# Kernel tuning notes

Hardware: AMD Instinct MI355X
Metric: run time of the kernel (lower is better)

The kernel has to match this reference:

```python
import jax, jax.numpy as jnp
import numpy as np

# dims
D_IN, D, H, HD = 1536, 256, 8, 32
DEPTH, FFN = 2, 1024
B, L = 1, 8191
NGRIDS, TILE = 256, 256
SEGMENTS = [1024, 2048, 4096, 8192, 16384]   # get_optimal_segment_length(32768, 256)
RATIOS = [1, 2, 4, 8, 16]                    # LongNet canonical dilation ratios
SCALE = HD ** -0.5


def setup_inputs() -> dict:
    key = jax.random.key(0)
    ks = jax.random.split(key, 16)
    w = lambda k, s: jax.random.normal(k, s, jnp.float32) * 0.02
    return {
        "x": jax.random.normal(ks[0], (B, L, D_IN), jnp.float32),
        "coords": jax.random.randint(ks[1], (B, L, 2), 0, NGRIDS * TILE, jnp.int32),
        "proj_w": w(ks[2], (D_IN, D)), "proj_b": jnp.zeros((D,), jnp.float32),
        "cls_tok": w(ks[3], (1, 1, D)),
        "Wq": w(ks[4], (DEPTH, D, D)), "Wk": w(ks[5], (DEPTH, D, D)),
        "Wv": w(ks[6], (DEPTH, D, D)), "Wo": w(ks[7], (DEPTH, D, D)),
        "bq": jnp.zeros((DEPTH, D), jnp.float32), "bk": jnp.zeros((DEPTH, D), jnp.float32),
        "bv": jnp.zeros((DEPTH, D), jnp.float32), "bo": jnp.zeros((DEPTH, D), jnp.float32),
        "ln1_g": jnp.ones((DEPTH, D), jnp.float32), "ln1_b": jnp.zeros((DEPTH, D), jnp.float32),
        "ln2_g": jnp.ones((DEPTH, D), jnp.float32), "ln2_b": jnp.zeros((DEPTH, D), jnp.float32),
        "W1": w(ks[8], (DEPTH, D, FFN)), "b1": jnp.zeros((DEPTH, FFN), jnp.float32),
        "W2": w(ks[9], (DEPTH, FFN, D)), "b2": jnp.zeros((DEPTH, D), jnp.float32),
        "enc_g": jnp.ones((D,), jnp.float32), "enc_b": jnp.zeros((D,), jnp.float32),
        "norm_g": jnp.ones((D,), jnp.float32), "norm_b": jnp.zeros((D,), jnp.float32),
    }


def _ln(x, g, b):
    mu = x.mean(-1, keepdims=True)
    v = ((x - mu) ** 2).mean(-1, keepdims=True)
    return (x - mu) * jax.lax.rsqrt(v + 1e-5) * g + b


def _pos_table():
    # MAE-style 2D sincos pos embed, row 0 = cls (zeros). [NGRIDS^2+1, D]
    g = jnp.arange(NGRIDS, dtype=jnp.float32)
    gw, gh = jnp.meshgrid(g, g)  # gw[i,j]=j, gh[i,j]=i; flatten index = i*NGRIDS + j
    def one(pos):
        omega = 1.0 / (10000.0 ** (jnp.arange(D // 4, dtype=jnp.float32) / (D // 4)))
        o = pos.reshape(-1)[:, None] * omega[None]
        return jnp.concatenate([jnp.sin(o), jnp.cos(o)], -1)
    tab = jnp.concatenate([one(gw), one(gh)], -1)
    return jnp.concatenate([jnp.zeros((1, D), jnp.float32), tab], 0)


def _dilated_attn(q, k, v):
    # q,k,v: [B,S,H,HD]. LongNet: per (segment w, dilation r) branch, sparse in-segment
    # attention on stride-r rows (head-dependent offset h%r), branches fused via their
    # softmax log-sum-exp weights.
    S = q.shape[1]
    hh = jnp.arange(H)[:, None]
    outs, lses = [], []
    for w, r in zip(SEGMENTS, RATIOS):
        n = (S + w - 1) // w
        Sp = n * w
        def seg(t):
            tp = jnp.pad(t, ((0, 0), (0, Sp - S), (0, 0), (0, 0)))
            return tp.reshape(B, n, w, H, HD).transpose(0, 1, 3, 2, 4)  # [B,n,H,w,HD]
        qs_, ks_, vs_ = seg(q), seg(k), seg(v)
        t = w // r
        idx = (hh % r) + r * jnp.arange(t)[None, :]                  # [H,t]
        qs = qs_[:, :, hh, idx]                                      # [B,n,H,t,HD]
        ks = ks_[:, :, hh, idx]
        vs = vs_[:, :, hh, idx]
        valid = (jnp.arange(n)[:, None, None] * w + idx[None]) < S   # [n,H,t]
        sc = jnp.einsum('bnhtd,bnhsd->bnhts', qs, ks) * SCALE
        sc = jnp.where(valid[None, :, :, None, :], sc, -1e9)
        m = sc.max(-1, keepdims=True)
        p = jnp.exp(sc - m)
        den = p.sum(-1, keepdims=True)
        o = jnp.einsum('bnhts,bnhsd->bnhtd', p, vs) / den
        lse = m[..., 0] + jnp.log(den[..., 0])                       # [B,n,H,t]
        fo = jnp.zeros((B, n, H, w, HD), q.dtype).at[:, :, hh, idx].set(o)
        fl = jnp.full((B, n, H, w), -1e30, q.dtype).at[:, :, hh, idx].set(lse)
        outs.append(fo.transpose(0, 1, 3, 2, 4).reshape(B, Sp, H, HD)[:, :S])
        lses.append(fl.transpose(0, 1, 3, 2).reshape(B, Sp, H)[:, :S])
    Ls = jnp.stack(lses)   # [5,B,S,H]
    Os = jnp.stack(outs)   # [5,B,S,H,HD]
    wts = jnp.exp(Ls - Ls.max(0, keepdims=True))
    return (wts[..., None] * Os).sum(0) / wts.sum(0)[..., None]


def _forward(x, coords, proj_w, proj_b, cls_tok, Wq, Wk, Wv, Wo, bq, bk, bv, bo,
             ln1_g, ln1_b, ln2_g, ln2_b, W1, b1, W2, b2, enc_g, enc_b, norm_g, norm_b):
    h = x @ proj_w + proj_b                                   # patch embed [B,L,D]
    tab = _pos_table()
    cg = jnp.floor(coords.astype(jnp.float32) / TILE).astype(jnp.int32)
    pos = cg[..., 0] * NGRIDS + cg[..., 1] + 1                # coords_to_pos
    h = h + tab[pos]
    cls = jnp.broadcast_to(cls_tok + tab[0], (B, 1, D))
    h = jnp.concatenate([cls, h], 1)                          # [B,S,D], S = L+1
    S = h.shape[1]
    for i in range(DEPTH):                                    # pre-LN LongNet encoder layers
        a = _ln(h, ln1_g[i], ln1_b[i])
        q = (a @ Wq[i] + bq[i]).reshape(B, S, H, HD)
        k = (a @ Wk[i] + bk[i]).reshape(B, S, H, HD)
        v = (a @ Wv[i] + bv[i]).reshape(B, S, H, HD)
        o = _dilated_attn(q, k, v).reshape(B, S, D)
        h = h + o @ Wo[i] + bo[i]
        f = _ln(h, ln2_g[i], ln2_b[i])
        h = h + jax.nn.gelu(f @ W1[i] + b1[i], approximate=False) @ W2[i] + b2[i]
    h = _ln(h, enc_g, enc_b)     # encoder final LN
    h = _ln(h, norm_g, norm_b)   # model self.norm
    return h[:, 0]               # cls embedding (global_pool=False)


def reference(x, coords, proj_w, proj_b, cls_tok, Wq, Wk, Wv, Wo, bq, bk, bv, bo,
              ln1_g, ln1_b, ln2_g, ln2_b, W1, b1, W2, b2, enc_g, enc_b, norm_g, norm_b):
    return _forward(x, coords, proj_w, proj_b, cls_tok, Wq, Wk, Wv, Wo, bq, bk, bv, bo,
                    ln1_g, ln1_b, ln2_g, ln2_b, W1, b1, W2, b2, enc_g, enc_b, norm_g, norm_b)
```

## Files before the change

### kernel.cpp

```cpp
#include <hip/hip_runtime.h>
#include <math.h>

#define S_TOT 8192
#define DD 256
#define NHEAD 8
#define HDSZ 32
#define ATT_SCALE 0.17677669529663687f
#define ATT_SCALE_LOG2E 0.25506601f

typedef short short8 __attribute__((ext_vector_type(8)));
typedef short short4v __attribute__((ext_vector_type(4)));
typedef float f32x4 __attribute__((ext_vector_type(4)));
typedef unsigned short ushort;

#define OFF_PROJ 0
#define OFF_WQ0  393216
#define OFF_WK0  458752
#define OFF_WV0  524288
#define OFF_WO0  589824
#define OFF_W10  655360
#define OFF_W20  917504
#define OFF_WK1  1179648
#define OFF_WV1  1245184
#define OFF_WQ1  1310720
// ... 131 lines not shown
void gemm4_kernel(const ushort* __restrict__ A, const ushort* __restrict__ Bt,
                  const float* __restrict__ bias, void* __restrict__ Cv,
                  int M, int N, int K, int flags, const int* __restrict__ coords)
{
    __shared__ ushort As[3][64][64];
    __shared__ ushort Bs[3][BN][64];
    constexpr int NT = BN / 32;
    const int nx  = N / BN;
    const int ny8 = gridDim.x / (8 * nx);
    const int b   = blockIdx.x;
    const int c8  = b & 7;
    const int j   = b >> 3;
    const int m0  = (c8 * ny8 + j / nx) * 64;
    const int n0  = (j % nx) * BN;

    const int tid  = threadIdx.x;
    const int wave = tid >> 6;
    const int lane = tid & 63;
    const int lrow = lane & 15;
    const int quad = lane >> 4;
    const int wr = (wave >> 1) * 32;
    const int wc = (wave & 1) * (BN / 2);

    float* Cf  = (float*)Cv;
    ushort* Cb = (ushort*)Cv;

    f32x4 acc[2][NT];
    #pragma unroll
    for (int mt = 0; mt < 2; ++mt)
        #pragma unroll
        for (int nt = 0; nt < NT; ++nt)
            acc[mt][nt] = (f32x4){0.f, 0.f, 0.f, 0.f};

    const int srow = tid >> 3;
    const int scol = (tid & 7) * 16;

    #define STAGE(BUF, KK)                                                        \
    do {                                                                          \
        _Pragma("unroll")                                                         \
        for (int c = 0; c < 2; ++c) {                                             \
            const int row = c * 32 + srow;                                        \
            const int sb  = scol ^ ((row & 7) << 4);                              \
            const ushort* srcp = A + (size_t)(m0 + row) * K + (KK) + (sb >> 1);   \
            __builtin_amdgcn_global_load_lds(                                     \
                (const __attribute__((address_space(1))) void*)srcp,              \
                (__attribute__((address_space(3))) void*)&As[BUF][c * 32 + wave * 8][0], \
                16, 0, 0);                                                        \
        }                                                                         \
        _Pragma("unroll")                                                         \
        for (int c = 0; c < BN / 32; ++c) {                                       \
            const int row = c * 32 + srow;                                        \
            const int sb  = scol ^ ((row & 7) << 4);                              \
            const ushort* srcp = Bt + (size_t)(n0 + row) * K + (KK) + (sb >> 1);  \
            __builtin_amdgcn_global_load_lds(                                     \
                (const __attribute__((address_space(1))) void*)srcp,              \
                (__attribute__((address_space(3))) void*)&Bs[BUF][c * 32 + wave * 8][0], \
                16, 0, 0);                                                        \
        }                                                                         \
    } while (0)

    #define COMPUTE(BUF)                                                          \
    do {                                                                          \
        _Pragma("unroll")                                                         \
        for (int ks = 0; ks < 2; ++ks) {                                          \
            short8 af[2], bfr[NT];                                                \
            _Pragma("unroll")                                                     \
            for (int mt = 0; mt < 2; ++mt) {                                      \
                const int row = wr + mt * 16 + lrow;                              \
                const int cb  = (ks * 64 + quad * 16) ^ ((row & 7) << 4);         \
                af[mt] = *(const short8*)((const char*)&As[BUF][row][0] + cb);    \
            }                                                                     \
            _Pragma("unroll")                                                     \
            for (int nt = 0; nt < NT; ++nt) {                                     \
                const int row = wc + nt * 16 + lrow;                              \
                const int cb  = (ks * 64 + quad * 16) ^ ((row & 7) << 4);         \
                bfr[nt] = *(const short8*)((const char*)&Bs[BUF][row][0] + cb);   \
            }                                                                     \
            _Pragma("unroll")                                                     \
            for (int mt = 0; mt < 2; ++mt)                                        \
                _Pragma("unroll")                                                 \
                for (int nt = 0; nt < NT; ++nt)                                   \
                    acc[mt][nt] = __builtin_amdgcn_mfma_f32_16x16x32_bf16(        \
                                      af[mt], bfr[nt], acc[mt][nt], 0, 0, 0);     \
        }                                                                         \
    } while (0)

    #define WAIT_BAR_N()                                                          \
    do {                                                                          \
        if constexpr (BN == 64) { asm volatile("s_waitcnt vmcnt(4)" ::: "memory"); } \
        else                    { asm volatile("s_waitcnt vmcnt(6)" ::: "memory"); } \
        __builtin_amdgcn_sched_barrier(0);                                        \
        __builtin_amdgcn_s_barrier();                                             \
        __builtin_amdgcn_sched_barrier(0);                                        \
    } while (0)

    #define WAIT_BAR_0()                                                          \
    do {                                                                          \
        asm volatile("s_waitcnt vmcnt(0)" ::: "memory");                          \
        __builtin_amdgcn_sched_barrier(0);                                        \
        __builtin_amdgcn_s_barrier();                                             \
        __builtin_amdgcn_sched_barrier(0);                                        \
    } while (0)

    const int ktiles = K >> 6;
    STAGE(0, 0);
    STAGE(1, 64);
    int bt = 0;
    for (int t = 0; t < ktiles - 2; ++t) {
        WAIT_BAR_N();
        const int nb = (bt + 2 >= 3) ? bt - 1 : bt + 2;
        STAGE(nb, (t + 2) * 64);
        COMPUTE(bt);
        bt = (bt + 1 == 3) ? 0 : bt + 1;
    }
    WAIT_BAR_N();
    COMPUTE(bt);
    bt = (bt + 1 == 3) ? 0 : bt + 1;
    WAIT_BAR_0();
    COMPUTE(bt);
    #undef STAGE
    #undef COMPUTE
    #undef WAIT_BAR_N
    #undef WAIT_BAR_0

    #pragma unroll
    for (int mt = 0; mt < 2; ++mt) {
        #pragma unroll
        for (int rg = 0; rg < 4; ++rg) {
            const int r = m0 + wr + mt * 16 + quad * 4 + rg;
            if (r >= M) continue;
            #pragma unroll
            for (int nt = 0; nt < NT; ++nt) {
                const int c = n0 + wc + nt * 16 + lrow;
                float vv = acc[mt][nt][rg] + bias[c];
                if (flags & 8) {
                    const int cg = coords[2 * r + ((c < 128) ? 1 : 0)] >> 8;
                    const float omega = exp2f((float)(c & 63) * -0.2076205059304703f);
                    const float o = (float)cg * omega;
                    vv += ((c & 64) == 0) ? __sinf(o) : __cosf(o);
                }
                if (flags & 16) { if (c < 256) vv *= ATT_SCALE_LOG2E; }
                if (flags & 2) vv = gelu_exact(vv);
                if (flags & 4) {
                    Cb[(size_t)r * N + c] = f2bf(vv);
                } else {
                    if (flags & 1) vv += Cf[(size_t)r * N + c];
                    Cf[(size_t)r * N + c] = vv;
                }
            }
        }
    }
}

__global__ __launch_bounds__(256)
void attn_mfma_kernel(const ushort* __restrict__ q, const ushort* __restrict__ k,
                      const ushort* __restrict__ v, float* __restrict__ bo5,
                      float* __restrict__ lse5, int qs)
{
    __shared__ ushort Kb[2][64][40];
    __shared__ ushort Vt[2][32][72];

    const int unit = blockIdx.x;
    const int segu = unit >> 3;
    const int head = unit & 7;
    int b2, n;
    if (segu < 8)        { b2 = 0; n = segu; }
    else if (segu < 12)  { b2 = 1; n = segu - 8; }
    else if (segu < 14)  { b2 = 2; n = segu - 12; }
    else if (segu == 14) { b2 = 3; n = 0; }
    else                 { b2 = 4; n = 0; }
    const int w  = 1024 << b2;
    const int rr = 1 << b2;
    const int base = n * w + (head & (rr - 1));

    int kEnd = (S_TOT - base + rr - 1) >> b2;
    if (kEnd > 1024) kEnd = 1024;
    if (blockIdx.y * 128 >= kEnd) return;

    const int tid  = threadIdx.x;
    const int wave = tid >> 6;
    const int lane = tid & 63;
    const int lrow = lane & 15;
    const int quad = lane >> 4;

    short8 qf[2];
    #pragma unroll
    for (int m = 0; m < 2; ++m) {
        const int j  = blockIdx.y * 128 + wave * 32 + m * 16 + lrow;
        const int pq = base + rr * j;
        qf[m] = *(const short8*)(q + (size_t)pq * qs + head * HDSZ + quad * 8);
    }

    f32x4 acc[2][2];
    float lsum[2] = {0.f, 0.f};
    #pragma unroll
    for (int m = 0; m < 2; ++m)
        #pragma unroll
        for (int dt = 0; dt < 2; ++dt) acc[m][dt] = (f32x4){0.f, 0.f, 0.f, 0.f};

    const int skr = tid >> 2;
    const int sdb = (tid & 3) * 8;
    const int grp = tid & 3;
    const int wcol = (2 * skr + 32 * grp) & 127;

    size_t prow = (size_t)(base + rr * skr) * qs + head * HDSZ + sdb;
    uint4 kreg = *(const uint4*)(k + prow);
    uint4 vreg = *(const uint4*)(v + prow);

    *(uint4*)&Kb[0][skr][sdb] = kreg;
    {
        const ushort* vp = (const ushort*)&vreg;
        #pragma unroll
        for (int i = 0; i < 8; ++i)
            *(ushort*)((char*)&Vt[0][sdb + i][0] + wcol) = vp[i];
    }

    int cur = 0;
    for (int kc = 0; kc < kEnd; kc += 64) {
        __syncthreads();
        const bool more = (kc + 64 < kEnd);
        if (more) {
            prow = (size_t)(base + rr * (kc + 64 + skr)) * qs + head * HDSZ + sdb;
            kreg = *(const uint4*)(k + prow);
            vreg = *(const uint4*)(v + prow);
        }

        short8 kf[4];
        #pragma unroll
        for (int t = 0; t < 4; ++t)
            kf[t] = *(const short8*)&Kb[cur][t * 16 + lrow][quad * 8];

        short8 vf[2][2];
        #pragma unroll
        for (int g = 0; g < 2; ++g)
            #pragma unroll
            for (int dt = 0; dt < 2; ++dt) {
                const int row  = dt * 16 + lrow;
                const int rotb = 32 * ((row >> 3) & 3);
                const int cb0  = (64 * g + 8 * quad + rotb) & 127;
                const int cb1  = (64 * g + 8 * quad + 32 + rotb) & 127;
                vf[g][dt] = cat44(*(const short4v*)((const char*)&Vt[cur][row][0] + cb0),
                                  *(const short4v*)((const char*)&Vt[cur][row][0] + cb1));
            }

        #pragma unroll
        for (int m = 0; m < 2; ++m) {
            f32x4 sc[4];
            #pragma unroll
            for (int t = 0; t < 4; ++t)
                sc[t] = __builtin_amdgcn_mfma_f32_16x16x32_bf16(
                            kf[t], qf[m], (f32x4){0.f,0.f,0.f,0.f}, 0, 0, 0);
            float p[4][4];
            #pragma unroll
            for (int t = 0; t < 4; ++t)
                #pragma unroll
                for (int rg = 0; rg < 4; ++rg)
                    p[t][rg] = exp2f(sc[t][rg]);
            float ps = 0.f;
            #pragma unroll
            for (int t = 0; t < 4; ++t)
                ps += (p[t][0] + p[t][1]) + (p[t][2] + p[t][3]);
            lsum[m] += ps;
            unsigned pw[4][2];
            #pragma unroll
            for (int t = 0; t < 4; ++t) {
                pw[t][0] = cvtpk_bf16(p[t][0], p[t][1]);
                pw[t][1] = cvtpk_bf16(p[t][2], p[t][3]);
            }
            #pragma unroll
            for (int g = 0; g < 2; ++g) {
                union { short8 s; unsigned u[4]; } pa;
                pa.u[0] = pw[2 * g][0];
                pa.u[1] = pw[2 * g][1];
                pa.u[2] = pw[2 * g + 1][0];
                pa.u[3] = pw[2 * g + 1][1];
                #pragma unroll
                for (int dt = 0; dt < 2; ++dt)
                    acc[m][dt] = __builtin_amdgcn_mfma_f32_16x16x32_bf16(
                                     pa.s, vf[g][dt], acc[m][dt], 0, 0, 0);
            }
        }

        if (more) {
            *(uint4*)&Kb[cur ^ 1][skr][sdb] = kreg;
            const ushort* vp = (const ushort*)&vreg;
            #pragma unroll
            for (int i = 0; i < 8; ++i)
                *(ushort*)((char*)&Vt[cur ^ 1][sdb + i][0] + wcol) = vp[i];
        }
        cur ^= 1;
    }

    #pragma unroll
    for (int m = 0; m < 2; ++m) {
        float tot = lsum[m];
        tot += __shfl_xor(tot, 16, 64);
        tot += __shfl_xor(tot, 32, 64);
        #pragma unroll
        for (int rg = 0; rg < 4; ++rg) {
            const float li = __shfl(tot, quad * 4 + rg, 16);
            const int j  = blockIdx.y * 128 + wave * 32 + m * 16 + quad * 4 + rg;
            const int pq = base + rr * j;
            const float inv = 1.0f / li;
            float* dst = bo5 + ((size_t)b2 * S_TOT + pq) * DD + head * HDSZ;
            dst[lrow]      = acc[m][0][rg] * inv;
            dst[16 + lrow] = acc[m][1][rg] * inv;
            if (lrow == 0)
                lse5[((size_t)b2 * S_TOT + pq) * NHEAD + head] = __logf(li);
        }
    }
}

__global__ __launch_bounds__(64)
void attn_row0_kernel(const float* __restrict__ q, const ushort* __restrict__ k,
                      const ushort* __restrict__ v, float* __restrict__ bo5,
                      float* __restrict__ lse5, int kvs)
{
    const int b2 = blockIdx.x >> 3;
    const int head = blockIdx.x & 7;
    const int r = 1 << b2;
    if (head & (r - 1)) return;
    const int tid = threadIdx.x;
    float qreg[32];
    #pragma unroll
    for (int d = 0; d < 32; d += 4) {
        const float4 t4 = *(const float4*)(q + head * HDSZ + d);
        qreg[d] = t4.x; qreg[d+1] = t4.y; qreg[d+2] = t4.z; qreg[d+3] = t4.w;
    }
    float m = -3.0e38f, l = 0.f, o[32];
    #pragma unroll
    for (int d = 0; d < 32; ++d) o[d] = 0.f;
    for (int j = tid; j < 1024; j += 64) {
        const int pk = r * j;
        float s;
        if (pk < S_TOT) {
            float s0 = 0.f;
            #pragma unroll
            for (int d = 0; d < 32; d += 8) {
                const uint4 raw = *(const uint4*)(k + (size_t)pk * kvs + head * HDSZ + d);
                const ushort* kp = (const ushort*)&raw;
                #pragma unroll
                for (int i = 0; i < 8; ++i) s0 += qreg[d + i] * bf2f(kp[i]);
            }
            s = s0 * ATT_SCALE;
        } else s = -1.0e9f;
        const float mn = fmaxf(m, s);
        const float c = __expf(m - mn);
        const float e = __expf(s - mn);
        l = l * c + e; m = mn;
        if (pk < S_TOT) {
            #pragma unroll
            for (int d = 0; d < 32; d += 8) {
                const uint4 raw = *(const uint4*)(v + (size_t)pk * kvs + head * HDSZ + d);
                const ushort* vp = (const ushort*)&raw;
                #pragma unroll
                for (int i = 0; i < 8; ++i) o[d + i] = o[d + i] * c + e * bf2f(vp[i]);
            }
        } else {
            #pragma unroll
            for (int d = 0; d < 32; ++d) o[d] *= c;
        }
    }
    __shared__ float ms[64], ls[64], os[64][32];
    ms[tid] = m; ls[tid] = l;
    #pragma unroll
    for (int d = 0; d < 32; ++d) os[tid][d] = o[d];
    __syncthreads();
    for (int st = 32; st >= 1; st >>= 1) {
        if (tid < st) {
            const float m2 = ms[tid + st], l2 = ls[tid + st];
            const float mn = fmaxf(ms[tid], m2);
            const float c1 = __expf(ms[tid] - mn);
            const float c2 = __expf(m2 - mn);
            ls[tid] = ls[tid] * c1 + l2 * c2;
            ms[tid] = mn;
            for (int d = 0; d < 32; ++d) os[tid][d] = os[tid][d]*c1 + os[tid+st][d]*c2;
        }
        __syncthreads();
    }
    if (tid < 32) bo5[(size_t)b2 * S_TOT * DD + head * HDSZ + tid] = os[0][tid] / ls[0];
    if (tid == 0) lse5[(size_t)b2 * S_TOT * NHEAD + head] = ms[0] + __logf(ls[0]);
}

__global__ __launch_bounds__(256)
void combine_kernel(const float* __restrict__ bo5, const float* __restrict__ lse5,
                    ushort* __restrict__ attn)
{
    const int p = blockIdx.x;
    const int d = threadIdx.x;
    const int h = d >> 5;
    float lse[5];
    bool sel[5];
    float mx = -3.0e38f;
    #pragma unroll
    for (int b2 = 0; b2 < 5; ++b2) {
        const int r = 1 << b2;
        sel[b2] = ((p & (r - 1)) == (h & (r - 1)));
        if (sel[b2]) {
            lse[b2] = lse5[((size_t)b2 * S_TOT + p) * NHEAD + h];
            mx = fmaxf(mx, lse[b2]);
        }
    }
    float wsum = 0.f, acc = 0.f;
    #pragma unroll
    for (int b2 = 0; b2 < 5; ++b2) {
        if (sel[b2]) {
            const float wgt = __expf(lse[b2] - mx);
            wsum += wgt;
            acc += wgt * bo5[((size_t)b2 * S_TOT + p) * DD + d];
        }
    }
    attn[(size_t)p * DD + d] = f2bf(acc / wsum);
}

__global__ __launch_bounds__(256)
void tail_qrow_kernel(const float* __restrict__ h, const float* __restrict__ g,
                      const float* __restrict__ b, const ushort* __restrict__ Wt,
                      const float* __restrict__ bias, float* __restrict__ qrow0)
{
    __shared__ float red[4];
    __shared__ float as[256];
    const int d = threadIdx.x;
    const float xv = h[d];
    const float mu = block_sum256(xv, red) * (1.0f / 256.0f);
    const float dv = xv - mu;
    const float var = block_sum256(dv * dv, red) * (1.0f / 256.0f);
    as[d] = dv * rsqrtf(var + 1e-5f) * g[d] + b[d];
    __syncthreads();
    float acc = 0.f;
    for (int k2 = 0; k2 < 256; k2 += 8) {
        const short8 w8 = *(const short8*)&Wt[(size_t)d * 256 + k2];
        #pragma unroll
        for (int j = 0; j < 8; ++j) acc += as[k2 + j] * bf2f((ushort)w8[j]);
    }
    qrow0[d] = acc + bias[d];
}

__global__ __launch_bounds__(256)
void tail_mid_kernel(const float* __restrict__ bo5, const float* __restrict__ lse5,
                     float* __restrict__ h, const ushort* __restrict__ Wo1t,
                     const float* __restrict__ bo1, const float* __restrict__ g2,
                     const float* __restrict__ b2, float* __restrict__ f)
{
    __shared__ float red[4];
    __shared__ float att[256];
    const int d = threadIdx.x;
    const int hh = d >> 5;
    float lse[5]; bool sel[5]; float mx = -3.0e38f;
    #pragma unroll
    for (int bb = 0; bb < 5; ++bb) {
        const int r = 1 << bb;
        sel[bb] = ((hh & (r - 1)) == 0);
        if (sel[bb]) {
            lse[bb] = lse5[(size_t)bb * S_TOT * NHEAD + hh];
            mx = fmaxf(mx, lse[bb]);
        }
    }
    float wsum = 0.f, acc = 0.f;
    #pragma unroll
    for (int bb = 0; bb < 5; ++bb) {
        if (sel[bb]) {
            const float wgt = __expf(lse[bb] - mx);
            wsum += wgt;
            acc += wgt * bo5[(size_t)bb * S_TOT * DD + d];
        }
    }
    att[d] = acc / wsum;
    __syncthreads();
    float a2 = 0.f;
    for (int k2 = 0; k2 < 256; k2 += 8) {
        const short8 w8 = *(const short8*)&Wo1t[(size_t)d * 256 + k2];
        #pragma unroll
        for (int j = 0; j < 8; ++j) a2 += att[k2 + j] * bf2f((ushort)w8[j]);
    }
    const float hv = a2 + bo1[d] + h[d];
    h[d] = hv;
    const float mu = block_sum256(hv, red) * (1.0f / 256.0f);
    const float dv = hv - mu;
    const float var = block_sum256(dv * dv, red) * (1.0f / 256.0f);
    f[d] = dv * rsqrtf(var + 1e-5f) * g2[d] + b2[d];
}

__global__ __launch_bounds__(256)
void tail_ffn1_kernel(const float* __restrict__ f, const ushort* __restrict__ W11t,
                      const float* __restrict__ b11, float* __restrict__ midr0)
{
    __shared__ float fs[256];
    const int tid = threadIdx.x;
    fs[tid] = f[tid];
    __syncthreads();
    const int n = blockIdx.x * 256 + tid;
    float acc = 0.f;
    for (int k2 = 0; k2 < 256; k2 += 8) {
        const short8 w8 = *(const short8*)&W11t[(size_t)n * 256 + k2];
        #pragma unroll
        for (int j = 0; j < 8; ++j) acc += fs[k2 + j] * bf2f((ushort)w8[j]);
    }
    midr0[n] = gelu_exact(acc + b11[n]);
}

__global__ __launch_bounds__(256)
void tail_ffn2_kernel(const float* __restrict__ midr0, const ushort* __restrict__ W21t,
                      const float* __restrict__ b21, float* __restrict__ h)
{
    __shared__ float ms[1024];
    const int tid = threadIdx.x;
    for (int i = tid; i < 1024; i += 256) ms[i] = midr0[i];
    __syncthreads();
    const int n  = blockIdx.x * 64 + (tid >> 2);
    const int kq = (tid & 3) * 256;
    float acc = 0.f;
    for (int k2 = 0; k2 < 256; k2 += 8) {
        const short8 w8 = *(const short8*)&W21t[(size_t)n * 1024 + kq + k2];
        #pragma unroll
        for (int j = 0; j < 8; ++j) acc += ms[kq + k2 + j] * bf2f((ushort)w8[j]);
    }
    acc += __shfl_xor(acc, 1);
    acc += __shfl_xor(acc, 2);
    if ((tid & 3) == 0) h[n] = h[n] + acc + b21[n];
}

__global__ __launch_bounds__(256)
void tail_final_kernel(const float* __restrict__ h, const float* __restrict__ eg,
                       const float* __restrict__ eb, const float* __restrict__ ng,
                       const float* __restrict__ nb, float* __restrict__ out)
{
    __shared__ float red[4];
    const int d = threadIdx.x;
    float xv = h[d];
    {
        const float mu = block_sum256(xv, red) * (1.0f / 256.0f);
        const float dv = xv - mu;
        const float var = block_sum256(dv * dv, red) * (1.0f / 256.0f);
        xv = dv * rsqrtf(var + 1e-5f) * eg[d] + eb[d];
    }
    {
        const float mu = block_sum256(xv, red) * (1.0f / 256.0f);
        const float dv = xv - mu;
        const float var = block_sum256(dv * dv, red) * (1.0f / 256.0f);
        out[d] = dv * rsqrtf(var + 1e-5f) * ng[d] + nb[d];
    }
}

extern "C" void kernel_launch(void* const* d_in, const int* in_sizes, int n_in,
                              void* d_out, int out_size, void* d_ws, size_t ws_size,
                              hipStream_t stream)
{
    const float* x      = (const float*)d_in[0];
    const int*   coords = (const int*)  d_in[1];
    const float* proj_w = (const float*)d_in[2];
    const float* proj_b = (const float*)d_in[3];
    const float* cls_tok= (const float*)d_in[4];
    const float* Wq     = (const float*)d_in[5];
    const float* Wk     = (const float*)d_in[6];
    const float* Wv     = (const float*)d_in[7];
    const float* Wo     = (const float*)d_in[8];
    const float* bq     = (const float*)d_in[9];
    const float* bk     = (const float*)d_in[10];
    const float* bv     = (const float*)d_in[11];
    const float* bo_    = (const float*)d_in[12];
    const float* ln1_g  = (const float*)d_in[13];
    const float* ln1_b  = (const float*)d_in[14];
    const float* ln2_g  = (const float*)d_in[15];
    const float* ln2_b  = (const float*)d_in[16];
    const float* W1     = (const float*)d_in[17];
    const float* b1     = (const float*)d_in[18];
    const float* W2     = (const float*)d_in[19];
    const float* b2v    = (const float*)d_in[20];
    const float* enc_g  = (const float*)d_in[21];
    const float* enc_b  = (const float*)d_in[22];
    const float* norm_g = (const float*)d_in[23];
    const float* norm_b = (const float*)d_in[24];
    float* out = (float*)d_out;

    const size_t SD = (size_t)S_TOT * DD;
    float* ws   = (float*)d_ws;
    float* h    = ws;
    float* big  = h + SD;
    float* bo5  = big;
    ushort* xbf   = (ushort*)big;
    ushort* midbf = (ushort*)big;
    float* lse5 = big + 5 * SD;
    ushort* a_bf    = (ushort*)(lse5 + 5 * S_TOT * NHEAD);
    ushort* qkv_bf  = a_bf + SD;
    ushort* attn_bf = qkv_bf + 3 * SD;
    ushort* wbuf    = attn_bf + SD;
    float* bqkv0  = (float*)(wbuf + WBUF_TOT);
    float* bkv1   = bqkv0 + 768;
    float* qrow0  = bkv1 + 512;
    float* f_r0   = qrow0 + 256;
    float* midr0  = f_r0 + 256;

    auto gemm64 = [&](const ushort* A, const ushort* Bt, const float* bias, void* C,
                      int M, int N, int K, int flags) {
        gemm4_kernel<64><<<128 * (N / 64), 256, 0, stream>>>(A, Bt, bias, C, M, N, K,
                                                             flags, coords);
    };
    auto gemm128 = [&](const ushort* A, const ushort* Bt, const float* bias, void* C,
                       int M, int N, int K, int flags) {
        gemm4_kernel<128><<<128 * (N / 128), 256, 0, stream>>>(A, Bt, bias, C, M, N, K,
                                                               flags, coords);
    };

    setup_kernel<<<6627, 256, 0, stream>>>(x, proj_w, Wq, Wk, Wv, Wo, W1, W2,
                                           bq, bk, bv, cls_tok, wbuf, bqkv0, bkv1,
                                           xbf, h);

    gemm64(xbf, wbuf + OFF_PROJ, proj_b, h + DD, 8191, 256, 1536, 8);

    ln_kernel<<<S_TOT / 4, 256, 0, stream>>>(h, ln1_g, ln1_b, a_bf);
    gemm128(a_bf, wbuf + OFF_WQ0, bqkv0, qkv_bf, 8192, 768, 256, 4 | 16);
    attn_mfma_kernel<<<dim3(128, 8), 256, 0, stream>>>(qkv_bf, qkv_bf + 256,
                                                       qkv_bf + 512, bo5, lse5, 768);
    combine_kernel<<<S_TOT, 256, 0, stream>>>(bo5, lse5, attn_bf);
    gemm64(attn_bf, wbuf + OFF_WO0, bo_, h, 8192, 256, 256, 1);
    ln_kernel<<<S_TOT / 4, 256, 0, stream>>>(h, ln2_g, ln2_b, a_bf);
    gemm128(a_bf, wbuf + OFF_W10, b1, midbf, 8192, 1024, 256, 4 | 2);
    gemm64(midbf, wbuf + OFF_W20, b2v, h, 8192, 256, 1024, 1);

    ln_kernel<<<S_TOT / 4, 256, 0, stream>>>(h, ln1_g + 256, ln1_b + 256, a_bf);
    gemm128(a_bf, wbuf + OFF_WK1, bkv1, qkv_bf, 8192, 512, 256, 4);
    tail_qrow_kernel<<<1, 256, 0, stream>>>(h, ln1_g + 256, ln1_b + 256,
                                            wbuf + OFF_WQ1, bq + 256, qrow0);
    attn_row0_kernel<<<40, 64, 0, stream>>>(qrow0, qkv_bf, qkv_bf + 256, bo5, lse5, 512);
    tail_mid_kernel<<<1, 256, 0, stream>>>(bo5, lse5, h, wbuf + OFF_WO1, bo_ + 256,
                                           ln2_g + 256, ln2_b + 256, f_r0);
    tail_ffn1_kernel<<<4, 256, 0, stream>>>(f_r0, wbuf + OFF_W11, b1 + 1024, midr0);
    tail_ffn2_kernel<<<4, 256, 0, stream>>>(midr0, wbuf + OFF_W21, b2v + 256, h);
    tail_final_kernel<<<1, 256, 0, stream>>>(h, enc_g, enc_b, norm_g, norm_b, out);
}
```

Measured before the change: 375.8 us.

## Split attention into single-wave blocks with register-staged K/V prefetch

The dilated attention kernel now runs one 64-thread wave per block covering 32 queries instead of four waves covering 128, so the grid is four times larger. Each block holds a single LDS K/V buffer and the per-chunk __syncthreads is replaced by explicit lgkmcnt waits and sched barriers; every lane loads four K/V rows into registers for the next chunk. The aim is more parallelism and no block-level barriers, at the cost of each block reloading K/V, which raises global memory traffic. The diff also adds a second setup_kernel launch, run first with bv passed in place of bk; it is redundant work that adds time and looks like a leftover.

```diff
diff --git a/kernel.cpp b/kernel.cpp
--- a/kernel.cpp
+++ b/kernel.cpp
@@ -307,13 +307,13 @@
     }
 }
 
-__global__ __launch_bounds__(256)
+__global__ __launch_bounds__(64)
 void attn_mfma_kernel(const ushort* __restrict__ q, const ushort* __restrict__ k,
                       const ushort* __restrict__ v, float* __restrict__ bo5,
                       float* __restrict__ lse5, int qs)
 {
-    __shared__ ushort Kb[2][64][40];
-    __shared__ ushort Vt[2][32][72];
+    __shared__ ushort Kb[64][40];
+    __shared__ ushort Vt[32][72];
 
     const int unit = blockIdx.x;
     const int segu = unit >> 3;
@@ -330,18 +330,16 @@
 
     int kEnd = (S_TOT - base + rr - 1) >> b2;
     if (kEnd > 1024) kEnd = 1024;
-    if (blockIdx.y * 128 >= kEnd) return;
-
-    const int tid  = threadIdx.x;
-    const int wave = tid >> 6;
-    const int lane = tid & 63;
+    if (blockIdx.y * 32 >= kEnd) return;
+
+    const int lane = threadIdx.x;
     const int lrow = lane & 15;
     const int quad = lane >> 4;
 
     short8 qf[2];
     #pragma unroll
     for (int m = 0; m < 2; ++m) {
-        const int j  = blockIdx.y * 128 + wave * 32 + m * 16 + lrow;
+        const int j  = blockIdx.y * 32 + m * 16 + lrow;
         const int pq = base + rr * j;
         qf[m] = *(const short8*)(q + (size_t)pq * qs + head * HDSZ + quad * 8);
     }
@@ -353,37 +351,36 @@
         #pragma unroll
         for (int dt = 0; dt < 2; ++dt) acc[m][dt] = (f32x4){0.f, 0.f, 0.f, 0.f};
 
-    const int skr = tid >> 2;
-    const int sdb = (tid & 3) * 8;
-    const int grp = tid & 3;
-    const int wcol = (2 * skr + 32 * grp) & 127;
-
-    size_t prow = (size_t)(base + rr * skr) * qs + head * HDSZ + sdb;
-    uint4 kreg = *(const uint4*)(k + prow);
-    uint4 vreg = *(const uint4*)(v + prow);
-
-    *(uint4*)&Kb[0][skr][sdb] = kreg;
-    {
-        const ushort* vp = (const ushort*)&vreg;
-        #pragma unroll
-        for (int i = 0; i < 8; ++i)
-            *(ushort*)((char*)&Vt[0][sdb + i][0] + wcol) = vp[i];
-    }
-
-    int cur = 0;
+    const int skr0 = lane >> 2;
+    const int sdb  = (lane & 3) * 8;
+    const int grp  = lane & 3;
+
+    uint4 kreg[4], vreg[4];
+    #pragma unroll
+    for (int i = 0; i < 4; ++i) {
+        const size_t prow = (size_t)(base + rr * (skr0 + 16 * i)) * qs + head * HDSZ + sdb;
+        kreg[i] = *(const uint4*)(k + prow);
+        vreg[i] = *(const uint4*)(v + prow);
+    }
+    #pragma unroll
+    for (int i = 0; i < 4; ++i) {
+        const int skr = skr0 + 16 * i;
+        *(uint4*)&Kb[skr][sdb] = kreg[i];
+        const int wcol = (2 * skr + 32 * grp) & 127;
+        const ushort* vp = (const ushort*)&vreg[i];
+        #pragma unroll
+        for (int jj = 0; jj < 8; ++jj)
+            *(ushort*)((char*)&Vt[sdb + jj][0] + wcol) = vp[jj];
+    }
+
     for (int kc = 0; kc < kEnd; kc += 64) {
-        __syncthreads();
-        const bool more = (kc + 64 < kEnd);
-        if (more) {
-            prow = (size_t)(base + rr * (kc + 64 + skr)) * qs + head * HDSZ + sdb;
-            kreg = *(const uint4*)(k + prow);
-            vreg = *(const uint4*)(v + prow);
-        }
+        asm volatile("s_waitcnt lgkmcnt(0)" ::: "memory");
+        __builtin_amdgcn_sched_barrier(0);
 
         short8 kf[4];
         #pragma unroll
         for (int t = 0; t < 4; ++t)
-            kf[t] = *(const short8*)&Kb[cur][t * 16 + lrow][quad * 8];
+            kf[t] = *(const short8*)&Kb[t * 16 + lrow][quad * 8];
 
         short8 vf[2][2];
         #pragma unroll
@@ -394,9 +391,22 @@
                 const int rotb = 32 * ((row >> 3) & 3);
                 const int cb0  = (64 * g + 8 * quad + rotb) & 127;
                 const int cb1  = (64 * g + 8 * quad + 32 + rotb) & 127;
-                vf[g][dt] = cat44(*(const short4v*)((const char*)&Vt[cur][row][0] + cb0),
-                                  *(const short4v*)((const char*)&Vt[cur][row][0] + cb1));
+                vf[g][dt] = cat44(*(const short4v*)((const char*)&Vt[row][0] + cb0),
+                                  *(const short4v*)((const char*)&Vt[row][0] + cb1));
             }
+        asm volatile("s_waitcnt lgkmcnt(0)" ::: "memory");
+        __builtin_amdgcn_sched_barrier(0);
+
+        const bool more = (kc + 64 < kEnd);
+        if (more) {
+            #pragma unroll
+            for (int i = 0; i < 4; ++i) {
+                const size_t prow = (size_t)(base + rr * (kc + 64 + skr0 + 16 * i)) * qs
+                                    + head * HDSZ + sdb;
+                kreg[i] = *(const uint4*)(k + prow);
+                vreg[i] = *(const uint4*)(v + prow);
+            }
+        }
 
         #pragma unroll
         for (int m = 0; m < 2; ++m) {
@@ -437,13 +447,17 @@
         }
 
         if (more) {
-            *(uint4*)&Kb[cur ^ 1][skr][sdb] = kreg;
-            const ushort* vp = (const ushort*)&vreg;
-            #pragma unroll
-            for (int i = 0; i < 8; ++i)
-                *(ushort*)((char*)&Vt[cur ^ 1][sdb + i][0] + wcol) = vp[i];
-        }
-        cur ^= 1;
+            #pragma unroll
+            for (int i = 0; i < 4; ++i) {
+                const int skr = skr0 + 16 * i;
+                *(uint4*)&Kb[skr][sdb] = kreg[i];
+                const int wcol = (2 * skr + 32 * grp) & 127;
+                const ushort* vp = (const ushort*)&vreg[i];
+                #pragma unroll
+                for (int jj = 0; jj < 8; ++jj)
+                    *(ushort*)((char*)&Vt[sdb + jj][0] + wcol) = vp[jj];
+            }
+        }
     }
 
     #pragma unroll
@@ -454,7 +468,7 @@
         #pragma unroll
         for (int rg = 0; rg < 4; ++rg) {
             const float li = __shfl(tot, quad * 4 + rg, 16);
-            const int j  = blockIdx.y * 128 + wave * 32 + m * 16 + quad * 4 + rg;
+            const int j  = blockIdx.y * 32 + m * 16 + quad * 4 + rg;
             const int pq = base + rr * j;
             const float inv = 1.0f / li;
             float* dst = bo5 + ((size_t)b2 * S_TOT + pq) * DD + head * HDSZ;
@@ -758,6 +772,9 @@
     };
 
     setup_kernel<<<6627, 256, 0, stream>>>(x, proj_w, Wq, Wk, Wv, Wo, W1, W2,
+                                           bq, bv, bv, cls_tok, wbuf, bqkv0, bkv1,
+                                           xbf, h);
+    setup_kernel<<<6627, 256, 0, stream>>>(x, proj_w, Wq, Wk, Wv, Wo, W1, W2,
                                            bq, bk, bv, cls_tok, wbuf, bqkv0, bkv1,
                                            xbf, h);
 
@@ -765,7 +782,7 @@
 
     ln_kernel<<<S_TOT / 4, 256, 0, stream>>>(h, ln1_g, ln1_b, a_bf);
     gemm128(a_bf, wbuf + OFF_WQ0, bqkv0, qkv_bf, 8192, 768, 256, 4 | 16);
-    attn_mfma_kernel<<<dim3(128, 8), 256, 0, stream>>>(qkv_bf, qkv_bf + 256,
+    attn_mfma_kernel<<<dim3(128, 32), 64, 0, stream>>>(qkv_bf, qkv_bf + 256,
                                                        qkv_bf + 512, bo5, lse5, 768);
     combine_kernel<<<S_TOT, 256, 0, stream>>>(bo5, lse5, attn_bf);
     gemm64(attn_bf, wbuf + OFF_WO0, bo_, h, 8192, 256, 256, 1);
```

Result: slower. 435.9 us (+16.0%).

## Fuse row-0 tail kernels into one block and use 64-wide GEMM tiles

Applied to the files above, without the earlier changes.

Replaces the six small row-0 tail launches (q projection, dilated attention for the cls row, output projection with LN, both FFN matmuls, final LNs) with a single 256-thread block that keeps intermediates in shared memory. The goal is to remove launch overhead and global round trips on a serial critical path. The cost is that the 40 attention units, which were spread over 40 blocks, now run on 4 waves of one block, four units each in sequence. That adds serial work, and a 34 KB shared array limits the kernel. Separately, the QKV, FFN1 and layer-1 KV GEMMs switch from 128-wide to 64-wide N tiles, giving more blocks per launch but less reuse of A per block.

```diff
diff --git a/kernel.cpp b/kernel.cpp
--- a/kernel.cpp
+++ b/kernel.cpp
@@ -466,77 +466,6 @@
     }
 }
 
-__global__ __launch_bounds__(64)
-void attn_row0_kernel(const float* __restrict__ q, const ushort* __restrict__ k,
-                      const ushort* __restrict__ v, float* __restrict__ bo5,
-                      float* __restrict__ lse5, int kvs)
-{
-    const int b2 = blockIdx.x >> 3;
-    const int head = blockIdx.x & 7;
-    const int r = 1 << b2;
-    if (head & (r - 1)) return;
-    const int tid = threadIdx.x;
-    float qreg[32];
-    #pragma unroll
-    for (int d = 0; d < 32; d += 4) {
-        const float4 t4 = *(const float4*)(q + head * HDSZ + d);
-        qreg[d] = t4.x; qreg[d+1] = t4.y; qreg[d+2] = t4.z; qreg[d+3] = t4.w;
-    }
-    float m = -3.0e38f, l = 0.f, o[32];
-    #pragma unroll
-    for (int d = 0; d < 32; ++d) o[d] = 0.f;
-    for (int j = tid; j < 1024; j += 64) {
-        const int pk = r * j;
-        float s;
-        if (pk < S_TOT) {
-            float s0 = 0.f;
-            #pragma unroll
-            for (int d = 0; d < 32; d += 8) {
-                const uint4 raw = *(const uint4*)(k + (size_t)pk * kvs + head * HDSZ + d);
-                const ushort* kp = (const ushort*)&raw;
-                #pragma unroll
-                for (int i = 0; i < 8; ++i) s0 += qreg[d + i] * bf2f(kp[i]);
-            }
-            s = s0 * ATT_SCALE;
-        } else s = -1.0e9f;
-        const float mn = fmaxf(m, s);
-        const float c = __expf(m - mn);
-        const float e = __expf(s - mn);
-        l = l * c + e; m = mn;
-        if (pk < S_TOT) {
-            #pragma unroll
-            for (int d = 0; d < 32; d += 8) {
-                const uint4 raw = *(const uint4*)(v + (size_t)pk * kvs + head * HDSZ + d);
-                const ushort* vp = (const ushort*)&raw;
-                #pragma unroll
-                for (int i = 0; i < 8; ++i) o[d + i] = o[d + i] * c + e * bf2f(vp[i]);
-            }
-        } else {
-            #pragma unroll
-            for (int d = 0; d < 32; ++d) o[d] *= c;
-        }
-    }
-    __shared__ float ms[64], ls[64], os[64][32];
-    ms[tid] = m; ls[tid] = l;
-    #pragma unroll
-    for (int d = 0; d < 32; ++d) os[tid][d] = o[d];
-    __syncthreads();
-    for (int st = 32; st >= 1; st >>= 1) {
-        if (tid < st) {
-            const float m2 = ms[tid + st], l2 = ls[tid + st];
-            const float mn = fmaxf(ms[tid], m2);
-            const float c1 = __expf(ms[tid] - mn);
-            const float c2 = __expf(m2 - mn);
-            ls[tid] = ls[tid] * c1 + l2 * c2;
-            ms[tid] = mn;
-            for (int d = 0; d < 32; ++d) os[tid][d] = os[tid][d]*c1 + os[tid+st][d]*c2;
-        }
-        __syncthreads();
-    }
-    if (tid < 32) bo5[(size_t)b2 * S_TOT * DD + head * HDSZ + tid] = os[0][tid] / ls[0];
-    if (tid == 0) lse5[(size_t)b2 * S_TOT * NHEAD + head] = ms[0] + __logf(ls[0]);
-}
-
 __global__ __launch_bounds__(256)
 void combine_kernel(const float* __restrict__ bo5, const float* __restrict__ lse5,
                     ushort* __restrict__ attn)
@@ -569,131 +498,206 @@
 }
 
 __global__ __launch_bounds__(256)
-void tail_qrow_kernel(const float* __restrict__ h, const float* __restrict__ g,
-                      const float* __restrict__ b, const ushort* __restrict__ Wt,
-                      const float* __restrict__ bias, float* __restrict__ qrow0)
+void tail_fused_kernel(const float* __restrict__ h,
+                       const float* __restrict__ g1, const float* __restrict__ b1l,
+                       const ushort* __restrict__ wbuf,
+                       const float* __restrict__ bq1,
+                       const ushort* __restrict__ kv,
+                       const float* __restrict__ bo1,
+                       const float* __restrict__ g2, const float* __restrict__ b2l,
+                       const float* __restrict__ b11, const float* __restrict__ b21,
+                       const float* __restrict__ eg, const float* __restrict__ eb,
+                       const float* __restrict__ ng, const float* __restrict__ nb,
+                       float* __restrict__ out)
 {
     __shared__ float red[4];
-    __shared__ float as[256];
-    const int d = threadIdx.x;
-    const float xv = h[d];
-    const float mu = block_sum256(xv, red) * (1.0f / 256.0f);
-    const float dv = xv - mu;
-    const float var = block_sum256(dv * dv, red) * (1.0f / 256.0f);
-    as[d] = dv * rsqrtf(var + 1e-5f) * g[d] + b[d];
-    __syncthreads();
-    float acc = 0.f;
-    for (int k2 = 0; k2 < 256; k2 += 8) {
-        const short8 w8 = *(const short8*)&Wt[(size_t)d * 256 + k2];
-        #pragma unroll
-        for (int j = 0; j < 8; ++j) acc += as[k2 + j] * bf2f((ushort)w8[j]);
-    }
-    qrow0[d] = acc + bias[d];
-}
-
-__global__ __launch_bounds__(256)
-void tail_mid_kernel(const float* __restrict__ bo5, const float* __restrict__ lse5,
-                     float* __restrict__ h, const ushort* __restrict__ Wo1t,
-                     const float* __restrict__ bo1, const float* __restrict__ g2,
-                     const float* __restrict__ b2, float* __restrict__ f)
-{
-    __shared__ float red[4];
-    __shared__ float att[256];
-    const int d = threadIdx.x;
-    const int hh = d >> 5;
-    float lse[5]; bool sel[5]; float mx = -3.0e38f;
-    #pragma unroll
-    for (int bb = 0; bb < 5; ++bb) {
-        const int r = 1 << bb;
-        sel[bb] = ((hh & (r - 1)) == 0);
-        if (sel[bb]) {
-            lse[bb] = lse5[(size_t)bb * S_TOT * NHEAD + hh];
-            mx = fmaxf(mx, lse[bb]);
-        }
-    }
-    float wsum = 0.f, acc = 0.f;
-    #pragma unroll
-    for (int bb = 0; bb < 5; ++bb) {
-        if (sel[bb]) {
-            const float wgt = __expf(lse[bb] - mx);
-            wsum += wgt;
-            acc += wgt * bo5[(size_t)bb * S_TOT * DD + d];
-        }
-    }
-    att[d] = acc / wsum;
-    __syncthreads();
-    float a2 = 0.f;
-    for (int k2 = 0; k2 < 256; k2 += 8) {
-        const short8 w8 = *(const short8*)&Wo1t[(size_t)d * 256 + k2];
-        #pragma unroll
-        for (int j = 0; j < 8; ++j) a2 += att[k2 + j] * bf2f((ushort)w8[j]);
-    }
-    const float hv = a2 + bo1[d] + h[d];
-    h[d] = hv;
-    const float mu = block_sum256(hv, red) * (1.0f / 256.0f);
-    const float dv = hv - mu;
-    const float var = block_sum256(dv * dv, red) * (1.0f / 256.0f);
-    f[d] = dv * rsqrtf(var + 1e-5f) * g2[d] + b2[d];
-}
-
-__global__ __launch_bounds__(256)
-void tail_ffn1_kernel(const float* __restrict__ f, const ushort* __restrict__ W11t,
-                      const float* __restrict__ b11, float* __restrict__ midr0)
-{
+    __shared__ float qrow_s[256];
+    __shared__ float bo_r0[5][256];
+    __shared__ float lse_r0[5][8];
     __shared__ float fs[256];
-    const int tid = threadIdx.x;
-    fs[tid] = f[tid];
-    __syncthreads();
-    const int n = blockIdx.x * 256 + tid;
-    float acc = 0.f;
-    for (int k2 = 0; k2 < 256; k2 += 8) {
-        const short8 w8 = *(const short8*)&W11t[(size_t)n * 256 + k2];
-        #pragma unroll
-        for (int j = 0; j < 8; ++j) acc += fs[k2 + j] * bf2f((ushort)w8[j]);
-    }
-    midr0[n] = gelu_exact(acc + b11[n]);
-}
-
-__global__ __launch_bounds__(256)
-void tail_ffn2_kernel(const float* __restrict__ midr0, const ushort* __restrict__ W21t,
-                      const float* __restrict__ b21, float* __restrict__ h)
-{
-    __shared__ float ms[1024];
-    const int tid = threadIdx.x;
-    for (int i = tid; i < 1024; i += 256) ms[i] = midr0[i];
-    __syncthreads();
-    const int n  = blockIdx.x * 64 + (tid >> 2);
-    const int kq = (tid & 3) * 256;
-    float acc = 0.f;
-    for (int k2 = 0; k2 < 256; k2 += 8) {
-        const short8 w8 = *(const short8*)&W21t[(size_t)n * 1024 + kq + k2];
-        #pragma unroll
-        for (int j = 0; j < 8; ++j) acc += ms[kq + k2 + j] * bf2f((ushort)w8[j]);
-    }
-    acc += __shfl_xor(acc, 1);
-    acc += __shfl_xor(acc, 2);
-    if ((tid & 3) == 0) h[n] = h[n] + acc + b21[n];
-}
-
-__global__ __launch_bounds__(256)
-void tail_final_kernel(const float* __restrict__ h, const float* __restrict__ eg,
-                       const float* __restrict__ eb, const float* __restrict__ ng,
-                       const float* __restrict__ nb, float* __restrict__ out)
-{
-    __shared__ float red[4];
-    const int d = threadIdx.x;
-    float xv = h[d];
+    __shared__ float ms1[1024];
+    __shared__ float hv_s[256];
+    __shared__ float ms2[4][64], ls2[4][64];
+    __shared__ float os2[4][64][32];
+
+    const int tid  = threadIdx.x;
+    const int wave = tid >> 6;
+    const int lane = tid & 63;
+
     {
+        const float xv = h[tid];
         const float mu = block_sum256(xv, red) * (1.0f / 256.0f);
         const float dv = xv - mu;
         const float var = block_sum256(dv * dv, red) * (1.0f / 256.0f);
-        xv = dv * rsqrtf(var + 1e-5f) * eg[d] + eb[d];
-    }
+        fs[tid] = dv * rsqrtf(var + 1e-5f) * g1[tid] + b1l[tid];
+        __syncthreads();
+        float acc = 0.f;
+        const ushort* Wt = wbuf + OFF_WQ1;
+        for (int k2 = 0; k2 < 256; k2 += 8) {
+            const short8 w8 = *(const short8*)&Wt[(size_t)tid * 256 + k2];
+            #pragma unroll
+            for (int j = 0; j < 8; ++j) acc += fs[k2 + j] * bf2f((ushort)w8[j]);
+        }
+        qrow_s[tid] = acc + bq1[tid];
+        __syncthreads();
+    }
+
+    for (int ui = 0; ui < 4; ++ui) {
+        const int u = wave * 4 + ui;
+        int b2, head;
+        if (u < 8)        { b2 = 0; head = u; }
+        else if (u < 12)  { b2 = 1; head = (u - 8) * 2; }
+        else if (u < 14)  { b2 = 2; head = (u - 12) * 4; }
+        else if (u == 14) { b2 = 3; head = 0; }
+        else              { b2 = 4; head = 0; }
+        const int r = 1 << b2;
+        float qreg[32];
+        #pragma unroll
+        for (int d = 0; d < 32; ++d) qreg[d] = qrow_s[head * 32 + d];
+        float m = -3.0e38f, l = 0.f, o[32];
+        #pragma unroll
+        for (int d = 0; d < 32; ++d) o[d] = 0.f;
+        for (int j = lane; j < 1024; j += 64) {
+            const int pk = r * j;
+            float s;
+            if (pk < S_TOT) {
+                float s0 = 0.f;
+                #pragma unroll
+                for (int d = 0; d < 32; d += 8) {
+                    const uint4 raw = *(const uint4*)(kv + (size_t)pk * 512 + head * 32 + d);
+                    const ushort* kp = (const ushort*)&raw;
+                    #pragma unroll
+                    for (int i = 0; i < 8; ++i) s0 += qreg[d + i] * bf2f(kp[i]);
+                }
+                s = s0 * ATT_SCALE;
+            } else s = -1.0e9f;
+            const float mn = fmaxf(m, s);
+            const float c = __expf(m - mn);
+            const float e = __expf(s - mn);
+            l = l * c + e; m = mn;
+            if (pk < S_TOT) {
+                #pragma unroll
+                for (int d = 0; d < 32; d += 8) {
+                    const uint4 raw = *(const uint4*)(kv + 256 + (size_t)pk * 512 + head * 32 + d);
+                    const ushort* vp = (const ushort*)&raw;
+                    #pragma unroll
+                    for (int i = 0; i < 8; ++i) o[d + i] = o[d + i] * c + e * bf2f(vp[i]);
+                }
+            } else {
+                #pragma unroll
+                for (int d = 0; d < 32; ++d) o[d] *= c;
+            }
+        }
+        ms2[wave][lane] = m; ls2[wave][lane] = l;
+        #pragma unroll
+        for (int d = 0; d < 32; ++d) os2[wave][lane][d] = o[d];
+        __syncthreads();
+        for (int st = 32; st >= 1; st >>= 1) {
+            if (lane < st) {
+                const float m2 = ms2[wave][lane + st], l2 = ls2[wave][lane + st];
+                const float mn = fmaxf(ms2[wave][lane], m2);
+                const float c1 = __expf(ms2[wave][lane] - mn);
+                const float c2 = __expf(m2 - mn);
+                ls2[wave][lane] = ls2[wave][lane] * c1 + l2 * c2;
+                ms2[wave][lane] = mn;
+                for (int d = 0; d < 32; ++d)
+                    os2[wave][lane][d] = os2[wave][lane][d] * c1 + os2[wave][lane + st][d] * c2;
+            }
+            __syncthreads();
+        }
+        if (lane < 32) bo_r0[b2][head * 32 + lane] = os2[wave][0][lane] / ls2[wave][0];
+        if (lane == 0) lse_r0[b2][head] = ms2[wave][0] + __logf(ls2[wave][0]);
+        __syncthreads();
+    }
+
+    float hv;
     {
-        const float mu = block_sum256(xv, red) * (1.0f / 256.0f);
-        const float dv = xv - mu;
+        const int hh = tid >> 5;
+        float lse[5]; bool sel[5]; float mx = -3.0e38f;
+        #pragma unroll
+        for (int bb = 0; bb < 5; ++bb) {
+            const int r = 1 << bb;
+            sel[bb] = ((hh & (r - 1)) == 0);
+            if (sel[bb]) {
+                lse[bb] = lse_r0[bb][hh];
+                mx = fmaxf(mx, lse[bb]);
+            }
+        }
+        float wsum = 0.f, acc = 0.f;
+        #pragma unroll
+        for (int bb = 0; bb < 5; ++bb) {
+            if (sel[bb]) {
+                const float wgt = __expf(lse[bb] - mx);
+                wsum += wgt;
+                acc += wgt * bo_r0[bb][tid];
+            }
+        }
+        fs[tid] = acc / wsum;
+        __syncthreads();
+        float a2 = 0.f;
+        const ushort* Wo1t = wbuf + OFF_WO1;
+        for (int k2 = 0; k2 < 256; k2 += 8) {
+            const short8 w8 = *(const short8*)&Wo1t[(size_t)tid * 256 + k2];
+            #pragma unroll
+            for (int j = 0; j < 8; ++j) a2 += fs[k2 + j] * bf2f((ushort)w8[j]);
+        }
+        hv = a2 + bo1[tid] + h[tid];
+        hv_s[tid] = hv;
+        const float mu = block_sum256(hv, red) * (1.0f / 256.0f);
+        const float dv = hv - mu;
         const float var = block_sum256(dv * dv, red) * (1.0f / 256.0f);
-        out[d] = dv * rsqrtf(var + 1e-5f) * ng[d] + nb[d];
+        __syncthreads();
+        fs[tid] = dv * rsqrtf(var + 1e-5f) * g2[tid] + b2l[tid];
+        __syncthreads();
+    }
+
+    {
+        const ushort* W11t = wbuf + OFF_W11;
+        for (int nn = 0; nn < 4; ++nn) {
+            const int n = nn * 256 + tid;
+            float acc = 0.f;
+            for (int k2 = 0; k2 < 256; k2 += 8) {
+                const short8 w8 = *(const short8*)&W11t[(size_t)n * 256 + k2];
+                #pragma unroll
+                for (int j = 0; j < 8; ++j) acc += fs[k2 + j] * bf2f((ushort)w8[j]);
+            }
+            ms1[n] = gelu_exact(acc + b11[n]);
+        }
+        __syncthreads();
+    }
+
+    {
+        const ushort* W21t = wbuf + OFF_W21;
+        for (int bb = 0; bb < 4; ++bb) {
+            const int n  = bb * 64 + (tid >> 2);
+            const int kq = (tid & 3) * 256;
+            float acc = 0.f;
+            for (int k2 = 0; k2 < 256; k2 += 8) {
+                const short8 w8 = *(const short8*)&W21t[(size_t)n * 1024 + kq + k2];
+                #pragma unroll
+                for (int j = 0; j < 8; ++j) acc += ms1[kq + k2 + j] * bf2f((ushort)w8[j]);
+            }
+            acc += __shfl_xor(acc, 1);
+            acc += __shfl_xor(acc, 2);
+            if ((tid & 3) == 0) hv_s[n] = hv_s[n] + acc + b21[n];
+        }
+        __syncthreads();
+    }
+
+    {
+        float xv = hv_s[tid];
+        {
+            const float mu = block_sum256(xv, red) * (1.0f / 256.0f);
+            const float dv = xv - mu;
+            const float var = block_sum256(dv * dv, red) * (1.0f / 256.0f);
+            xv = dv * rsqrtf(var + 1e-5f) * eg[tid] + eb[tid];
+        }
+        {
+            const float mu = block_sum256(xv, red) * (1.0f / 256.0f);
+            const float dv = xv - mu;
+            const float var = block_sum256(dv * dv, red) * (1.0f / 256.0f);
+            out[tid] = dv * rsqrtf(var + 1e-5f) * ng[tid] + nb[tid];
+        }
     }
 }
 
@@ -742,20 +746,12 @@
     ushort* wbuf    = attn_bf + SD;
     float* bqkv0  = (float*)(wbuf + WBUF_TOT);
     float* bkv1   = bqkv0 + 768;
-    float* qrow0  = bkv1 + 512;
-    float* f_r0   = qrow0 + 256;
-    float* midr0  = f_r0 + 256;
 
     auto gemm64 = [&](const ushort* A, const ushort* Bt, const float* bias, void* C,
                       int M, int N, int K, int flags) {
         gemm4_kernel<64><<<128 * (N / 64), 256, 0, stream>>>(A, Bt, bias, C, M, N, K,
                                                              flags, coords);
     };
-    auto gemm128 = [&](const ushort* A, const ushort* Bt, const float* bias, void* C,
-                       int M, int N, int K, int flags) {
-        gemm4_kernel<128><<<128 * (N / 128), 256, 0, stream>>>(A, Bt, bias, C, M, N, K,
-                                                               flags, coords);
-    };
 
     setup_kernel<<<6627, 256, 0, stream>>>(x, proj_w, Wq, Wk, Wv, Wo, W1, W2,
                                            bq, bk, bv, cls_tok, wbuf, bqkv0, bkv1,
@@ -764,23 +760,20 @@
     gemm64(xbf, wbuf + OFF_PROJ, proj_b, h + DD, 8191, 256, 1536, 8);
 
     ln_kernel<<<S_TOT / 4, 256, 0, stream>>>(h, ln1_g, ln1_b, a_bf);
-    gemm128(a_bf, wbuf + OFF_WQ0, bqkv0, qkv_bf, 8192, 768, 256, 4 | 16);
+    gemm64(a_bf, wbuf + OFF_WQ0, bqkv0, qkv_bf, 8192, 768, 256, 4 | 16);
     attn_mfma_kernel<<<dim3(128, 8), 256, 0, stream>>>(qkv_bf, qkv_bf + 256,
                                                        qkv_bf + 512, bo5, lse5, 768);
     combine_kernel<<<S_TOT, 256, 0, stream>>>(bo5, lse5, attn_bf);
     gemm64(attn_bf, wbuf + OFF_WO0, bo_, h, 8192, 256, 256, 1);
     ln_kernel<<<S_TOT / 4, 256, 0, stream>>>(h, ln2_g, ln2_b, a_bf);
-    gemm128(a_bf, wbuf + OFF_W10, b1, midbf, 8192, 1024, 256, 4 | 2);
+    gemm64(a_bf, wbuf + OFF_W10, b1, midbf, 8192, 1024, 256, 4 | 2);
     gemm64(midbf, wbuf + OFF_W20, b2v, h, 8192, 256, 1024, 1);
 
     ln_kernel<<<S_TOT / 4, 256, 0, stream>>>(h, ln1_g + 256, ln1_b + 256, a_bf);
-    gemm128(a_bf, wbuf + OFF_WK1, bkv1, qkv_bf, 8192, 512, 256, 4);
-    tail_qrow_kernel<<<1, 256, 0, stream>>>(h, ln1_g + 256, ln1_b + 256,
-                                            wbuf + OFF_WQ1, bq + 256, qrow0);
-    attn_row0_kernel<<<40, 64, 0, stream>>>(qrow0, qkv_bf, qkv_bf + 256, bo5, lse5, 512);
-    tail_mid_kernel<<<1, 256, 0, stream>>>(bo5, lse5, h, wbuf + OFF_WO1, bo_ + 256,
-                                           ln2_g + 256, ln2_b + 256, f_r0);
-    tail_ffn1_kernel<<<4, 256, 0, stream>>>(f_r0, wbuf + OFF_W11, b1 + 1024, midr0);
-    tail_ffn2_kernel<<<4, 256, 0, stream>>>(midr0, wbuf + OFF_W21, b2v + 256, h);
-    tail_final_kernel<<<1, 256, 0, stream>>>(h, enc_g, enc_b, norm_g, norm_b, out);
-}
+    gemm64(a_bf, wbuf + OFF_WK1, bkv1, qkv_bf, 8192, 512, 256, 4);
+    tail_fused_kernel<<<1, 256, 0, stream>>>(h, ln1_g + 256, ln1_b + 256, wbuf,
+                                             bq + 256, qkv_bf, bo_ + 256,
+                                             ln2_g + 256, ln2_b + 256,
+                                             b1 + 1024, b2v + 256,
+                                             enc_g, enc_b, norm_g, norm_b, out);
+}
```

Result: slower. 463.0 us (+23.2%).
